# Optimization experiments

Hardware: AMD Instinct MI355X
Metric: run time of the kernel (lower is better)

## Reference

```python
import jax, jax.numpy as jnp
import numpy as np

CH = 64          # channels
OC = 64          # out_channels
B, H, W = 8, 128, 128
NCA_C = CH + OC  # 128, NCA state channels
K = 3            # kernel_size
DILS = (1, 2, 4, 8)
HID = 64         # NCA update hidden
EPS = 1e-5


def setup_inputs() -> dict:
    key = jax.random.key(0)
    ks = jax.random.split(key, 16)
    def n(k, shape, s=0.02):
        return jax.random.normal(k, shape, jnp.float32) * s
    return {
        "x": jax.random.normal(ks[0], (B, H, W, CH), jnp.float32),
        "c": jax.random.normal(ks[1], (B, OC), jnp.float32),
        # Attention params
        "Wq": n(ks[2], (CH, OC)), "bq": jnp.zeros((OC,), jnp.float32),
        "Wk": n(ks[3], (OC, OC)), "bk": jnp.zeros((OC,), jnp.float32),
        "Wv": n(ks[4], (OC, OC)), "bv": jnp.zeros((OC,), jnp.float32),
        "Wo": n(ks[5], (OC, OC)), "bo": jnp.zeros((OC,), jnp.float32),
        "ln_g": jnp.ones((OC,), jnp.float32), "ln_b": jnp.zeros((OC,), jnp.float32),
        # NCA depthwise perception kernels, one per dilation: [4, NCA_C, 1, K, K]
        "pk": n(ks[6], (len(DILS), NCA_C, 1, K, K), 0.1),
        # NCA update MLP
        "W1": n(ks[7], ((1 + len(DILS)) * NCA_C, HID)), "b1": jnp.zeros((HID,), jnp.float32),
        "W2": n(ks[8], (HID, CH)), "b2": jnp.zeros((CH,), jnp.float32),
    }


def _layernorm(z, g, b):
    m = jnp.mean(z, axis=-1, keepdims=True)
    v = jnp.var(z, axis=-1, keepdims=True)
    return (z - m) / jnp.sqrt(v + EPS) * g + b


def _forward(x, c, Wq, bq, Wk, bk, Wv, bv, Wo, bo, ln_g, ln_b, pk, W1, b1, W2, b2):
    b_, h_, w_, _ = x.shape
    # ---- Attention(x, c): single-key softmax pooling over H*W ----
    q = x.reshape(b_, h_ * w_, CH) @ Wq + bq              # [B, HW, OC]
    k = c @ Wk + bk                                        # [B, OC]
    v = c @ Wv + bv                                        # [B, OC]
    scores = jnp.einsum('bno,bo->bn', q, k) * (OC ** -0.5)  # [B, HW]
    attn = jax.nn.softmax(scores, axis=1)                  # softmax over spatial dim
    attended = jnp.einsum('bn,bo->bo', attn, v)            # weighted pool (weights sum to 1)
    a = _layernorm(attended @ Wo + bo + c, ln_g, ln_b)     # out_proj + residual + LN
    c2 = c + a                                             # outer residual in NCAAttention

    # ---- concat broadcast context -> NCA state [B,H,W,NCA_C] ----
    c_exp = jnp.broadcast_to(c2[:, None, None, :], (b_, h_, w_, OC))
    xc = jnp.concatenate([x, c_exp], axis=-1)

    # ---- NCA perception: depthwise dilated convs (SAME padding) ----
    xp = jnp.transpose(xc, (0, 3, 1, 2))                   # NCHW
    feats = [xc]
    for i, d in enumerate(DILS):
        pad = d * (K // 2)
        p = jax.lax.conv_general_dilated(
            xp, pk[i], window_strides=(1, 1),
            padding=[(pad, pad), (pad, pad)], rhs_dilation=(d, d),
            dimension_numbers=('NCHW', 'OIHW', 'NCHW'),
            feature_group_count=NCA_C)
        feats.append(jnp.transpose(p, (0, 2, 3, 1)))
    upd_in = jnp.concatenate(feats, axis=-1)               # [B,H,W,5*NCA_C]

    # ---- NCA update MLP: Linear -> (Dropout=id) -> GELU -> Linear ----
    hidden = jax.nn.gelu(upd_in @ W1 + b1, approximate=False)
    y = hidden @ W2 + b2                                   # [B,H,W,CH]
    # NCA.out_channels (64) != NCA.channels (128) -> no residual add
    return y, c2


def reference(x, c, Wq, bq, Wk, bk, Wv, bv, Wo, bo, ln_g, ln_b, pk, W1, b1, W2, b2):
    return _forward(x, c, Wq, bq, Wk, bk, Wv, bv, Wo, bo, ln_g, ln_b, pk, W1, b1, W2, b2)
```

## Files before the change

kernel.cpp:

```cpp
#include <hip/hip_runtime.h>
#include <hip/hip_bf16.h>
#include <math.h>


typedef float  f32x4 __attribute__((ext_vector_type(4)));
typedef short  s16x8 __attribute__((ext_vector_type(8)));
typedef long   i64x2 __attribute__((ext_vector_type(2)));

static __device__ __forceinline__ unsigned short f2bf(float f) {
    __hip_bfloat16 h = __float2bfloat16(f);
    unsigned short u; __builtin_memcpy(&u, &h, 2); return u;
}
static __device__ __forceinline__ unsigned pk4fp8(float f0, float f1, float f2, float f3) {
    int v = 0;
    v = __builtin_amdgcn_cvt_pk_fp8_f32(f0, f1, v, false);
    v = __builtin_amdgcn_cvt_pk_fp8_f32(f2, f3, v, true);
    return (unsigned)v;
}

#define XROWB  9216
#define XBATCH 1327104
#define USCALE 256.0f

__global__ void prep2(const float* __restrict__ x,  const float* __restrict__ pk,
                      const float* __restrict__ W1, const float* __restrict__ W2,
                      const float* __restrict__ b1,
                      const float* __restrict__ c,
                      const float* __restrict__ Wv, const float* __restrict__ bv,
                      const float* __restrict__ Wo, const float* __restrict__ bo,
                      const float* __restrict__ lng, const float* __restrict__ lnb,
                      unsigned char* __restrict__ xp, unsigned char* __restrict__ Uf,
                      unsigned short* __restrict__ W2s,
                      float* __restrict__ V, float* __restrict__ hcp,
                      float* __restrict__ outc2)
{
    const int blk = blockIdx.x, tid = threadIdx.x;
    __shared__ float sc[512], sv[512], c2s[512];

    if (blk >= 683) {
        sc[tid] = c[tid]; sc[tid + 256] = c[tid + 256];
        __syncthreads();
        #pragma unroll
        for (int half = 0; half < 2; ++half) {
            int it = tid + half*256;
            int bb = it >> 6, j = it & 63;
            float v = bv[j];
            for (int i = 0; i < 64; ++i) v += sc[bb*64 + i]*Wv[i*64 + j];
            sv[it] = v;
        }
        __syncthreads();
        #pragma unroll
        for (int half = 0; half < 2; ++half) {
            int it = tid + half*256;
            int bb = it >> 6, j = it & 63;
            float t = bo[j] + sc[it];
            for (int i = 0; i < 64; ++i) t += sv[bb*64 + i]*Wo[i*64 + j];
            float s = t;
            for (int o = 32; o > 0; o >>= 1) s += __shfl_xor(s, o);
            float m = s * (1.f/64.f);
            float dq = (t - m)*(t - m);
            for (int o = 32; o > 0; o >>= 1) dq += __shfl_xor(dq, o);
            float a = (t - m) / sqrtf(dq*(1.f/64.f) + 1e-5f) * lng[j] + lnb[j];
            c2s[it] = sc[it] + a;
        }
        __syncthreads();
    }

    if (blk < 512) {
        int i = blk*256 + tid;
        int xc = i & 127, y = (i >> 7) & 127, b = i >> 14;
        const float* src = x + (size_t)i*64;
        float4 f[16];
        #pragma unroll
        for (int k = 0; k < 16; ++k) f[k] = *(const float4*)(src + k*4);
        unsigned P[16];
        #pragma unroll
        for (int k = 0; k < 16; ++k) P[k] = pk4fp8(f[k].x, f[k].y, f[k].z, f[k].w);
        unsigned char* d = xp + (size_t)b*XBATCH + (size_t)(y+8)*XROWB + (size_t)(xc+8)*64;
        *(uint4*)(d +  0) = make_uint4(P[0], P[1], P[8],  P[9]);
        *(uint4*)(d + 16) = make_uint4(P[2], P[3], P[10], P[11]);
        *(uint4*)(d + 32) = make_uint4(P[4], P[5], P[12], P[13]);
        *(uint4*)(d + 48) = make_uint4(P[6], P[7], P[14], P[15]);
    } else if (blk < 648) {
        int idx = (blk - 512)*256 + tid;
        int b = idx / 4352, r = idx - b*4352;
        int yy, xx;
        if (r < 2304) { int ry = r / 144; xx = r - ry*144; yy = (ry < 8) ? ry : 128 + ry; }
        else { int r2 = r - 2304; yy = 8 + (r2 >> 4); int xi = r2 & 15; xx = (xi < 8) ? xi : 128 + xi; }
        unsigned char* d = xp + (size_t)b*XBATCH + (size_t)yy*XROWB + (size_t)xx*64;
        uint4 z = make_uint4(0,0,0,0);
        *(uint4*)(d) = z; *(uint4*)(d+16) = z; *(uint4*)(d+32) = z; *(uint4*)(d+48) = z;
    } else if (blk < 681) {
        int idx = (blk - 648)*256 + tid;
        if (idx < 8448) {
            int lane = idx & 63, nt = (idx >> 6) & 3, pos = idx >> 8;
            int n  = nt*16 + (lane & 15);
            static constexpr int DI[33] = {3,3,3, 2,2,2, 1,1,1, 0,0,0, -1, 0,0, 1,1, 2,2, 3,3,
                                           0,0,0, 1,1,1, 2,2,2, 3,3,3};
            static constexpr int TT[33] = {0,1,2, 0,1,2, 0,1,2, 0,1,2, 4, 3,5, 3,5, 3,5, 3,5,
                                           6,7,8, 6,7,8, 6,7,8, 6,7,8};
            int di = DI[pos], t = TT[pos];
            float vv[16];
            #pragma unroll
            for (int kc2 = 0; kc2 < 2; ++kc2)
                #pragma unroll
                for (int j = 0; j < 8; ++j) {
                    int ch = kc2*32 + (lane >> 4)*8 + j;
                    float v;
                    if (di < 0) {
                        v = W1[ch*64 + n];
                        for (int dd = 0; dd < 4; ++dd)
                            v += pk[(dd*128 + ch)*9 + 4] * W1[((1+dd)*128 + ch)*64 + n];
                    } else {
                        v = pk[(di*128 + ch)*9 + t] * W1[((1+di)*128 + ch)*64 + n];
                    }
                    vv[kc2*8 + j] = v * USCALE;
                }
            uint4 o;
            o.x = pk4fp8(vv[0],  vv[1],  vv[2],  vv[3]);
            o.y = pk4fp8(vv[4],  vv[5],  vv[6],  vv[7]);
            o.z = pk4fp8(vv[8],  vv[9],  vv[10], vv[11]);
            o.w = pk4fp8(vv[12], vv[13], vv[14], vv[15]);
            *(uint4*)(Uf + (size_t)idx*16) = o;
        }
    } else if (blk < 683) {
        int idx = (blk - 681)*256 + tid;
        int lane = idx & 63, nt = (idx >> 6) & 3, kc2 = (idx >> 8) & 1;
        int n  = nt*16 + (lane & 15);
        int k0 = kc2*32 + (lane >> 4)*8;
        unsigned short e[8];
        #pragma unroll
        for (int j = 0; j < 8; ++j) e[j] = f2bf(W2[(k0+j)*64 + n]);
        uint4 o;
        o.x = (unsigned)e[0] | ((unsigned)e[1] << 16);
        o.y = (unsigned)e[2] | ((unsigned)e[3] << 16);
        o.z = (unsigned)e[4] | ((unsigned)e[5] << 16);
        o.w = (unsigned)e[6] | ((unsigned)e[7] << 16);
        *(uint4*)(W2s + (size_t)idx*8) = o;
    } else if (blk < 755) {
        int idx = (blk - 683)*256 + tid;
        int n = idx & 63, q = idx >> 6;
        int p = q % 36, b = q / 36;
        int di = p/9, t = p%9;
        float s = 0.f;
        for (int j = 0; j < 64; ++j)
            s += c2s[b*64 + j] * pk[(di*128 + 64 + j)*9 + t] * W1[((1+di)*128 + 64 + j)*64 + n];
        V[(size_t)q*64 + n] = s;
    } else {
        for (int it = tid; it < 512; it += 256) {
            int b = it >> 6, n = it & 63;
            float s = b1[n];
            for (int j = 0; j < 64; ++j) s += c2s[b*64 + j]*W1[(64 + j)*64 + n];
            hcp[it] = s;
            if (blk == 755) outc2[it] = c2s[it];
        }
    }
}

#define HID_S 72

__global__ __launch_bounds__(512, 4) void nca_main(
    const unsigned char* __restrict__ xp,
    const unsigned char* __restrict__ U,
    const unsigned short* __restrict__ W2s,
    const float* __restrict__ V,
    const float* __restrict__ hcp,
    const float* __restrict__ b2,
    float* __restrict__ out)
{
    __shared__ __align__(16) unsigned char smem[36864];
    __shared__ float V_l[36*64];
    __shared__ float Cx_l[16*64];
    __shared__ float Cy_l[2*64];
    __shared__ float hc2_l[64];

    unsigned short* hid = (unsigned short*)smem;

    const int tid = threadIdx.x;
    const int blk = blockIdx.x;
    const int b  = blk & 7;
    const int y0 = (blk >> 3) * 2;

    #pragma unroll
    for (int s = 0; s < 2; ++s) {
        int off = tid*16 + s*8192;
        __builtin_amdgcn_global_load_lds(
            (const __attribute__((address_space(1))) unsigned int*)(U + off),
            (__attribute__((address_space(3))) unsigned int*)(smem + off),
            16, 0, 0);
    }

    {
        const float4* Vg = (const float4*)(V + (size_t)b*2304);
        for (int i = tid; i < 576; i += 512) ((float4*)V_l)[i] = Vg[i];
    }
    __syncthreads();
    for (int it = tid; it < 1024; it += 512) {
        int xi = it >> 6, n = it & 63;
        int xx = xi < 8 ? xi : 112 + xi;
        float s = 0.f;
        #pragma unroll
        for (int di = 0; di < 4; ++di) {
            int d = 1 << di;
            int dxo = (xx < d) ? 0 : ((xx >= 128 - d) ? 2 : -1);
            if (dxo >= 0) {
                s += V_l[(di*9 + 0*3 + dxo)*64 + n];
                s += V_l[(di*9 + 1*3 + dxo)*64 + n];
                s += V_l[(di*9 + 2*3 + dxo)*64 + n];
            }
        }
        Cx_l[it] = s;
    }
    if (tid < 128) {
        int r = tid >> 6, n = tid & 63;
        int yy = y0 + r;
        float s = 0.f;
        #pragma unroll
        for (int di = 0; di < 4; ++di) {
            int d = 1 << di;
            int dyo = (yy < d) ? 0 : ((yy >= 128 - d) ? 2 : -1);
            if (dyo >= 0) {
                s += V_l[(di*9 + dyo*3 + 0)*64 + n];
                s += V_l[(di*9 + dyo*3 + 1)*64 + n];
                s += V_l[(di*9 + dyo*3 + 2)*64 + n];
            }
        }
        Cy_l[tid] = s;
    } else if (tid < 192) {
        int n = tid - 128;
        float s = hcp[b*64 + n];
        for (int p = 0; p < 36; ++p) s += V_l[p*64 + n];
        hc2_l[n] = s;
    }
    __syncthreads();

    const int lane = tid & 63;
    const int w    = tid >> 6;
    const int rib  = w >> 2;
    const int y    = y0 + rib;
    const int xw   = (w & 3) * 32;
    const int ln15 = lane & 15;
    const int oct  = lane >> 4;

    const unsigned char* abase = xp + (size_t)b*XBATCH + (size_t)(y + 8)*XROWB
                               + (size_t)(xw + ln15 + 8)*64 + oct*16;

    f32x4 acc[2][4];
    #pragma unroll
    for (int mt = 0; mt < 2; ++mt)
        #pragma unroll
        for (int nt = 0; nt < 4; ++nt) {
            acc[mt][nt][0] = 0.f; acc[mt][nt][1] = 0.f;
            acc[mt][nt][2] = 0.f; acc[mt][nt][3] = 0.f;
        }

    static constexpr int OFF[33] = {
        (-8*144-8)*64, (-8*144)*64, (-8*144+8)*64,
        (-4*144-4)*64, (-4*144)*64, (-4*144+4)*64,
        (-2*144-2)*64, (-2*144)*64, (-2*144+2)*64,
        (-1*144-1)*64, (-1*144)*64, (-1*144+1)*64,
        0,
        -64, 64, -128, 128, -256, 256, -512, 512,
        ( 1*144-1)*64, ( 1*144)*64, ( 1*144+1)*64,
        ( 2*144-2)*64, ( 2*144)*64, ( 2*144+2)*64,
        ( 4*144-4)*64, ( 4*144)*64, ( 4*144+4)*64,
        ( 8*144-8)*64, ( 8*144)*64, ( 8*144+8)*64
    };

    auto loadA = [&](int pos, i64x2* A) {
        const unsigned char* rp = abase + OFF[pos];
        A[0] = *(const i64x2*)(rp);
        A[1] = *(const i64x2*)(rp + 1024);
    };
    auto loadB = [&](int bufofs, int p, i64x2* Bv) {
        const unsigned char* rp = smem + bufofs + p*4096 + lane*16;
        #pragma unroll
        for (int nt = 0; nt < 4; ++nt) Bv[nt] = *(const i64x2*)(rp + nt*1024);
    };
    auto mfma_step = [&](const i64x2* A, const i64x2* Bv) {
        #pragma unroll
        for (int kc2 = 0; kc2 < 2; ++kc2)
            #pragma unroll
            for (int nt = 0; nt < 4; ++nt) {
                long bfr = Bv[nt][kc2];
                #pragma unroll
                for (int mt = 0; mt < 2; ++mt)
                    acc[mt][nt] = __builtin_amdgcn_mfma_f32_16x16x32_fp8_fp8(A[mt][kc2], bfr, acc[mt][nt], 0, 0, 0);
            }
    };

    i64x2 Areg[2][2], Breg[2][4];
    loadA(0, Areg[0]);
    loadB(0, 0, Breg[0]);

    int cur = 0;
    #pragma unroll 1
    for (int kb = 0; kb < 8; ++kb) {
        {
            const int nbytes = (kb < 7) ? 16384 : 4096;
            const unsigned char* gsrc = U + (size_t)(kb + 1)*16384;
            unsigned char* ldst = smem + (cur ^ 1)*16384;
            for (int off = tid*16; off < nbytes; off += 8192)
                __builtin_amdgcn_global_load_lds(
                    (const __attribute__((address_space(1))) unsigned int*)(gsrc + off),
                    (__attribute__((address_space(3))) unsigned int*)(ldst + off),
                    16, 0, 0);
        }
        const int cofs = cur*16384;
        #pragma unroll
        for (int p = 0; p < 4; ++p) {
            const int pos = kb*4 + p;
            loadA(pos + 1, Areg[(p + 1) & 1]);
            if (p < 3) loadB(cofs, p + 1, Breg[(p + 1) & 1]);
            __builtin_amdgcn_s_setprio(1);
            mfma_step(Areg[p & 1], Breg[p & 1]);
            __builtin_amdgcn_s_setprio(0);
        }
        __syncthreads();
        cur ^= 1;
        loadB(cur*16384, 0, Breg[0]);
    }
    __builtin_amdgcn_s_setprio(1);
    mfma_step(Areg[0], Breg[0]);
    __builtin_amdgcn_s_setprio(0);
    __syncthreads();

    const bool yedge = (y < 8) || (y >= 120);
    #pragma unroll
    for (int mt = 0; mt < 2; ++mt) {
        #pragma unroll
        for (int nt = 0; nt < 4; ++nt) {
            const int n = nt*16 + ln15;
            const float hcv = hc2_l[n];
            const float cyv = yedge ? Cy_l[rib*64 + n] : 0.f;
            #pragma unroll
            for (int r = 0; r < 4; ++r) {
                int m = oct*4 + r;
                int x = xw + mt*16 + m;
                float h = acc[mt][nt][r]*(1.0f/USCALE) + hcv - cyv;
                if (x < 8 || x >= 120) {
                    int xi = (x < 8) ? x : (x - 112);
                    h -= Cx_l[xi*64 + n];
                    if (yedge) {
                        #pragma unroll
                        for (int di = 0; di < 4; ++di) {
                            int d = 1 << di;
                            int dyo = (y < d) ? 0 : ((y >= 128 - d) ? 2 : -1);
                            int dxo = (x < d) ? 0 : ((x >= 128 - d) ? 2 : -1);
                            if (dyo >= 0 && dxo >= 0)
                                h += V_l[(di*9 + dyo*3 + dxo)*64 + n];
                        }
                    }
                }
                float u = 0.7978845608028654f * (h + 0.044715f*h*h*h);
                float g = h / (1.f + __expf(-2.f*u));
                hid[(rib*128 + x)*HID_S + n] = f2bf(g);
            }
        }
    }

    f32x4 acc2[2][4];
    #pragma unroll
    for (int mt = 0; mt < 2; ++mt)
        #pragma unroll
        for (int nt = 0; nt < 4; ++nt) {
            acc2[mt][nt][0] = 0.f; acc2[mt][nt][1] = 0.f;
            acc2[mt][nt][2] = 0.f; acc2[mt][nt][3] = 0.f;
        }
    #pragma unroll
    for (int kc2 = 0; kc2 < 2; ++kc2) {
        s16x8 a2[2];
        #pragma unroll
        for (int mt = 0; mt < 2; ++mt)
            a2[mt] = *(const s16x8*)&hid[(rib*128 + xw + mt*16 + ln15)*HID_S + kc2*32 + oct*8];
        #pragma unroll
        for (int nt = 0; nt < 4; ++nt) {
            s16x8 bfr = *(const s16x8*)(W2s + ((size_t)(kc2*4 + nt)*64 + lane)*8);
            #pragma unroll
            for (int mt = 0; mt < 2; ++mt)
                acc2[mt][nt] = __builtin_amdgcn_mfma_f32_16x16x32_bf16(a2[mt], bfr, acc2[mt][nt], 0, 0, 0);
        }
    }

    float* ob = out + ((size_t)(b*128 + y))*128*64;
    #pragma unroll
    for (int nt = 0; nt < 4; ++nt) {
        const float b2v = b2[nt*16 + ln15];
        #pragma unroll
        for (int mt = 0; mt < 2; ++mt) {
            #pragma unroll
            for (int r = 0; r < 4; ++r) {
                int x = xw + mt*16 + oct*4 + r;
                ob[(size_t)x*64 + nt*16 + ln15] = acc2[mt][nt][r] + b2v;
            }
        }
    }
}

extern "C" void kernel_launch(void* const* d_in, const int* in_sizes, int n_in,
                              void* d_out, int out_size, void* d_ws, size_t ws_size,
                              hipStream_t stream) {
    const float* x   = (const float*)d_in[0];
    const float* c   = (const float*)d_in[1];
    const float* Wv  = (const float*)d_in[6];
    const float* bv  = (const float*)d_in[7];
    const float* Wo  = (const float*)d_in[8];
    const float* bo  = (const float*)d_in[9];
    const float* lng = (const float*)d_in[10];
    const float* lnb = (const float*)d_in[11];
    const float* pk  = (const float*)d_in[12];
    const float* W1  = (const float*)d_in[13];
    const float* b1  = (const float*)d_in[14];
    const float* W2  = (const float*)d_in[15];
    const float* b2  = (const float*)d_in[16];
    float* out = (float*)d_out;

    char* w = (char*)d_ws;
    unsigned char*  xpb = (unsigned char*)(w);
    unsigned char*  Uf  = (unsigned char*)(w + 10616832);
    unsigned short* W2s = (unsigned short*)(w + 10752000);
    float*          V   = (float*)         (w + 10760192);
    float*          hcp = (float*)         (w + 10833920);

    prep2<<<757, 256, 0, stream>>>(x, pk, W1, W2, b1, c, Wv, bv, Wo, bo, lng, lnb,
                                   xpb, Uf, W2s, V, hcp, out + 8388608);
    nca_main<<<512, 512, 0, stream>>>(xpb, Uf, W2s, V, hcp, b2, out);
}
```

Measured before the change: 154.5 us.

## Switch NCA main GEMM to 32x32x64 scaled FP8 MFMA with repacked weights

Replaces the 16x16x32 fp8 MFMA tiles in the first MLP GEMM with the gfx950 32x32x64 f8f6f4 scaled MFMA. The weight U is repacked in the prep kernel for the new operand layout, and the LDS double buffer grows to 32KB stages so the K loop runs 4 iterations instead of 8. The activation staging is changed to coalesced per-channel-group writes. The intent is fewer MFMA issues and fewer LDS/global load instructions per FLOP. In exchange, the larger LDS footprint (64KB) may reduce occupancy.

```diff
diff --git a/kernel.cpp b/kernel.cpp
--- a/kernel.cpp
+++ b/kernel.cpp
@@ -3,9 +3,11 @@
 #include <math.h>
 
 
-typedef float  f32x4 __attribute__((ext_vector_type(4)));
-typedef short  s16x8 __attribute__((ext_vector_type(8)));
-typedef long   i64x2 __attribute__((ext_vector_type(2)));
+typedef float  f32x4  __attribute__((ext_vector_type(4)));
+typedef float  f32x16 __attribute__((ext_vector_type(16)));
+typedef short  s16x8  __attribute__((ext_vector_type(8)));
+typedef int    i32x4  __attribute__((ext_vector_type(4)));
+typedef int    i32x8  __attribute__((ext_vector_type(8)));
 
 static __device__ __forceinline__ unsigned short f2bf(float f) {
     __hip_bfloat16 h = __float2bfloat16(f);
@@ -37,7 +39,7 @@
     const int blk = blockIdx.x, tid = threadIdx.x;
     __shared__ float sc[512], sv[512], c2s[512];
 
-    if (blk >= 683) {
+    if (blk >= 667) {
         sc[tid] = c[tid]; sc[tid + 256] = c[tid + 256];
         __syncthreads();
         #pragma unroll
@@ -67,20 +69,16 @@
     }
 
     if (blk < 512) {
-        int i = blk*256 + tid;
-        int xc = i & 127, y = (i >> 7) & 127, b = i >> 14;
-        const float* src = x + (size_t)i*64;
-        float4 f[16];
-        #pragma unroll
-        for (int k = 0; k < 16; ++k) f[k] = *(const float4*)(src + k*4);
-        unsigned P[16];
-        #pragma unroll
-        for (int k = 0; k < 16; ++k) P[k] = pk4fp8(f[k].x, f[k].y, f[k].z, f[k].w);
-        unsigned char* d = xp + (size_t)b*XBATCH + (size_t)(y+8)*XROWB + (size_t)(xc+8)*64;
-        *(uint4*)(d +  0) = make_uint4(P[0], P[1], P[8],  P[9]);
-        *(uint4*)(d + 16) = make_uint4(P[2], P[3], P[10], P[11]);
-        *(uint4*)(d + 32) = make_uint4(P[4], P[5], P[12], P[13]);
-        *(uint4*)(d + 48) = make_uint4(P[6], P[7], P[14], P[15]);
+        const int ci = tid & 15;
+        #pragma unroll 4
+        for (int it = 0; it < 16; ++it) {
+            int px = blk*256 + it*16 + (tid >> 4);
+            int xc = px & 127, y = (px >> 7) & 127, b = px >> 14;
+            float4 f = *(const float4*)(x + (size_t)px*64 + ci*4);
+            unsigned P = pk4fp8(f.x, f.y, f.z, f.w);
+            *(unsigned*)(xp + (size_t)b*XBATCH + (size_t)(y+8)*XROWB
+                            + (size_t)(xc+8)*64 + ci*4) = P;
+        }
     } else if (blk < 648) {
         int idx = (blk - 512)*256 + tid;
         int b = idx / 4352, r = idx - b*4352;
@@ -90,41 +88,46 @@
         unsigned char* d = xp + (size_t)b*XBATCH + (size_t)yy*XROWB + (size_t)xx*64;
         uint4 z = make_uint4(0,0,0,0);
         *(uint4*)(d) = z; *(uint4*)(d+16) = z; *(uint4*)(d+32) = z; *(uint4*)(d+48) = z;
-    } else if (blk < 681) {
+    } else if (blk < 665) {
         int idx = (blk - 648)*256 + tid;
-        if (idx < 8448) {
-            int lane = idx & 63, nt = (idx >> 6) & 3, pos = idx >> 8;
-            int n  = nt*16 + (lane & 15);
+        if (idx < 4224) {
+            int lane = idx & 63, nt = (idx >> 6) & 1, pos = idx >> 7;
+            int n  = nt*32 + (lane & 31);
+            int h  = lane >> 5;
             static constexpr int DI[33] = {3,3,3, 2,2,2, 1,1,1, 0,0,0, -1, 0,0, 1,1, 2,2, 3,3,
                                            0,0,0, 1,1,1, 2,2,2, 3,3,3};
             static constexpr int TT[33] = {0,1,2, 0,1,2, 0,1,2, 0,1,2, 4, 3,5, 3,5, 3,5, 3,5,
                                            6,7,8, 6,7,8, 6,7,8, 6,7,8};
             int di = DI[pos], t = TT[pos];
-            float vv[16];
+            float vv[32];
             #pragma unroll
-            for (int kc2 = 0; kc2 < 2; ++kc2)
-                #pragma unroll
-                for (int j = 0; j < 8; ++j) {
-                    int ch = kc2*32 + (lane >> 4)*8 + j;
-                    float v;
-                    if (di < 0) {
-                        v = W1[ch*64 + n];
-                        for (int dd = 0; dd < 4; ++dd)
-                            v += pk[(dd*128 + ch)*9 + 4] * W1[((1+dd)*128 + ch)*64 + n];
-                    } else {
-                        v = pk[(di*128 + ch)*9 + t] * W1[((1+di)*128 + ch)*64 + n];
-                    }
-                    vv[kc2*8 + j] = v * USCALE;
+            for (int j = 0; j < 32; ++j) {
+                int ch = h*32 + j;
+                float v;
+                if (di < 0) {
+                    v = W1[ch*64 + n];
+                    for (int dd = 0; dd < 4; ++dd)
+                        v += pk[(dd*128 + ch)*9 + 4] * W1[((1+dd)*128 + ch)*64 + n];
+                } else {
+                    v = pk[(di*128 + ch)*9 + t] * W1[((1+di)*128 + ch)*64 + n];
                 }
-            uint4 o;
-            o.x = pk4fp8(vv[0],  vv[1],  vv[2],  vv[3]);
-            o.y = pk4fp8(vv[4],  vv[5],  vv[6],  vv[7]);
-            o.z = pk4fp8(vv[8],  vv[9],  vv[10], vv[11]);
-            o.w = pk4fp8(vv[12], vv[13], vv[14], vv[15]);
-            *(uint4*)(Uf + (size_t)idx*16) = o;
-        }
-    } else if (blk < 683) {
-        int idx = (blk - 681)*256 + tid;
+                vv[j] = v * USCALE;
+            }
+            unsigned char* base = Uf + (size_t)pos*4096 + nt*2048 + lane*16;
+            uint4 o0, o1;
+            o0.x = pk4fp8(vv[0],  vv[1],  vv[2],  vv[3]);
+            o0.y = pk4fp8(vv[4],  vv[5],  vv[6],  vv[7]);
+            o0.z = pk4fp8(vv[8],  vv[9],  vv[10], vv[11]);
+            o0.w = pk4fp8(vv[12], vv[13], vv[14], vv[15]);
+            o1.x = pk4fp8(vv[16], vv[17], vv[18], vv[19]);
+            o1.y = pk4fp8(vv[20], vv[21], vv[22], vv[23]);
+            o1.z = pk4fp8(vv[24], vv[25], vv[26], vv[27]);
+            o1.w = pk4fp8(vv[28], vv[29], vv[30], vv[31]);
+            *(uint4*)(base)        = o0;
+            *(uint4*)(base + 1024) = o1;
+        }
+    } else if (blk < 667) {
+        int idx = (blk - 665)*256 + tid;
         int lane = idx & 63, nt = (idx >> 6) & 3, kc2 = (idx >> 8) & 1;
         int n  = nt*16 + (lane & 15);
         int k0 = kc2*32 + (lane >> 4)*8;
@@ -137,8 +140,8 @@
         o.z = (unsigned)e[4] | ((unsigned)e[5] << 16);
         o.w = (unsigned)e[6] | ((unsigned)e[7] << 16);
         *(uint4*)(W2s + (size_t)idx*8) = o;
-    } else if (blk < 755) {
-        int idx = (blk - 683)*256 + tid;
+    } else if (blk < 739) {
+        int idx = (blk - 667)*256 + tid;
         int n = idx & 63, q = idx >> 6;
         int p = q % 36, b = q / 36;
         int di = p/9, t = p%9;
@@ -152,7 +155,7 @@
             float s = b1[n];
             for (int j = 0; j < 64; ++j) s += c2s[b*64 + j]*W1[(64 + j)*64 + n];
             hcp[it] = s;
-            if (blk == 755) outc2[it] = c2s[it];
+            outc2[it] = c2s[it];
         }
     }
 }
@@ -168,7 +171,7 @@
     const float* __restrict__ b2,
     float* __restrict__ out)
 {
-    __shared__ __align__(16) unsigned char smem[36864];
+    __shared__ __align__(16) unsigned char smem[65536];
     __shared__ float V_l[36*64];
     __shared__ float Cx_l[16*64];
     __shared__ float Cy_l[2*64];
@@ -182,7 +185,7 @@
     const int y0 = (blk >> 3) * 2;
 
     #pragma unroll
-    for (int s = 0; s < 2; ++s) {
+    for (int s = 0; s < 4; ++s) {
         int off = tid*16 + s*8192;
         __builtin_amdgcn_global_load_lds(
             (const __attribute__((address_space(1))) unsigned int*)(U + off),
@@ -241,18 +244,17 @@
     const int xw   = (w & 3) * 32;
     const int ln15 = lane & 15;
     const int oct  = lane >> 4;
+    const int l31  = lane & 31;
+    const int kg   = lane >> 5;
 
     const unsigned char* abase = xp + (size_t)b*XBATCH + (size_t)(y + 8)*XROWB
-                               + (size_t)(xw + ln15 + 8)*64 + oct*16;
-
-    f32x4 acc[2][4];
-    #pragma unroll
-    for (int mt = 0; mt < 2; ++mt)
-        #pragma unroll
-        for (int nt = 0; nt < 4; ++nt) {
-            acc[mt][nt][0] = 0.f; acc[mt][nt][1] = 0.f;
-            acc[mt][nt][2] = 0.f; acc[mt][nt][3] = 0.f;
-        }
+                               + (size_t)(xw + l31 + 8)*64 + kg*32;
+
+    f32x16 acc[2];
+    #pragma unroll
+    for (int nt = 0; nt < 2; ++nt)
+        #pragma unroll
+        for (int r = 0; r < 16; ++r) acc[nt][r] = 0.f;
 
     static constexpr int OFF[33] = {
         (-8*144-8)*64, (-8*144)*64, (-8*144+8)*64,
@@ -267,95 +269,90 @@
         ( 8*144-8)*64, ( 8*144)*64, ( 8*144+8)*64
     };
 
-    auto loadA = [&](int pos, i64x2* A) {
-        const unsigned char* rp = abase + OFF[pos];
-        A[0] = *(const i64x2*)(rp);
-        A[1] = *(const i64x2*)(rp + 1024);
+    auto loadB = [&](int cofs, int p, i32x8* Bv) {
+        const unsigned char* rp = smem + cofs + p*4096 + lane*16;
+        #pragma unroll
+        for (int nt = 0; nt < 2; ++nt) {
+            i32x4 lo = *(const i32x4*)(rp + nt*2048);
+            i32x4 hi = *(const i32x4*)(rp + nt*2048 + 1024);
+            i32x8 v;
+            v[0]=lo[0]; v[1]=lo[1]; v[2]=lo[2]; v[3]=lo[3];
+            v[4]=hi[0]; v[5]=hi[1]; v[6]=hi[2]; v[7]=hi[3];
+            Bv[nt] = v;
+        }
     };
-    auto loadB = [&](int bufofs, int p, i64x2* Bv) {
-        const unsigned char* rp = smem + bufofs + p*4096 + lane*16;
-        #pragma unroll
-        for (int nt = 0; nt < 4; ++nt) Bv[nt] = *(const i64x2*)(rp + nt*1024);
-    };
-    auto mfma_step = [&](const i64x2* A, const i64x2* Bv) {
-        #pragma unroll
-        for (int kc2 = 0; kc2 < 2; ++kc2)
-            #pragma unroll
-            for (int nt = 0; nt < 4; ++nt) {
-                long bfr = Bv[nt][kc2];
-                #pragma unroll
-                for (int mt = 0; mt < 2; ++mt)
-                    acc[mt][nt] = __builtin_amdgcn_mfma_f32_16x16x32_fp8_fp8(A[mt][kc2], bfr, acc[mt][nt], 0, 0, 0);
-            }
-    };
-
-    i64x2 Areg[2][2], Breg[2][4];
-    loadA(0, Areg[0]);
+
+    i32x8 Areg[2];
+    i32x8 Breg[2][2];
+    Areg[0] = *(const i32x8*)(abase + OFF[0]);
     loadB(0, 0, Breg[0]);
 
     int cur = 0;
     #pragma unroll 1
-    for (int kb = 0; kb < 8; ++kb) {
+    for (int kb = 0; kb < 4; ++kb) {
         {
-            const int nbytes = (kb < 7) ? 16384 : 4096;
-            const unsigned char* gsrc = U + (size_t)(kb + 1)*16384;
-            unsigned char* ldst = smem + (cur ^ 1)*16384;
+            const int nbytes = (kb < 3) ? 32768 : 4096;
+            const unsigned char* gsrc = U + (size_t)(kb + 1)*32768;
+            unsigned char* ldst = smem + (cur ^ 1)*32768;
             for (int off = tid*16; off < nbytes; off += 8192)
                 __builtin_amdgcn_global_load_lds(
                     (const __attribute__((address_space(1))) unsigned int*)(gsrc + off),
                     (__attribute__((address_space(3))) unsigned int*)(ldst + off),
                     16, 0, 0);
         }
-        const int cofs = cur*16384;
-        #pragma unroll
-        for (int p = 0; p < 4; ++p) {
-            const int pos = kb*4 + p;
-            loadA(pos + 1, Areg[(p + 1) & 1]);
-            if (p < 3) loadB(cofs, p + 1, Breg[(p + 1) & 1]);
+        const int cofs = cur*32768;
+        #pragma unroll
+        for (int p = 0; p < 8; ++p) {
+            const int pos = kb*8 + p;
+            Areg[(p + 1) & 1] = *(const i32x8*)(abase + OFF[pos + 1]);
+            if (p < 7) loadB(cofs, p + 1, Breg[(p + 1) & 1]);
             __builtin_amdgcn_s_setprio(1);
-            mfma_step(Areg[p & 1], Breg[p & 1]);
+            acc[0] = __builtin_amdgcn_mfma_scale_f32_32x32x64_f8f6f4(
+                Areg[p & 1], Breg[p & 1][0], acc[0], 0, 0, 0, 0x7F7F7F7F, 0, 0x7F7F7F7F);
+            acc[1] = __builtin_amdgcn_mfma_scale_f32_32x32x64_f8f6f4(
+                Areg[p & 1], Breg[p & 1][1], acc[1], 0, 0, 0, 0x7F7F7F7F, 0, 0x7F7F7F7F);
             __builtin_amdgcn_s_setprio(0);
         }
         __syncthreads();
         cur ^= 1;
-        loadB(cur*16384, 0, Breg[0]);
+        loadB(cur*32768, 0, Breg[0]);
     }
     __builtin_amdgcn_s_setprio(1);
-    mfma_step(Areg[0], Breg[0]);
+    acc[0] = __builtin_amdgcn_mfma_scale_f32_32x32x64_f8f6f4(
+        Areg[0], Breg[0][0], acc[0], 0, 0, 0, 0x7F7F7F7F, 0, 0x7F7F7F7F);
+    acc[1] = __builtin_amdgcn_mfma_scale_f32_32x32x64_f8f6f4(
+        Areg[0], Breg[0][1], acc[1], 0, 0, 0, 0x7F7F7F7F, 0, 0x7F7F7F7F);
     __builtin_amdgcn_s_setprio(0);
     __syncthreads();
 
     const bool yedge = (y < 8) || (y >= 120);
     #pragma unroll
-    for (int mt = 0; mt < 2; ++mt) {
-        #pragma unroll
-        for (int nt = 0; nt < 4; ++nt) {
-            const int n = nt*16 + ln15;
-            const float hcv = hc2_l[n];
-            const float cyv = yedge ? Cy_l[rib*64 + n] : 0.f;
-            #pragma unroll
-            for (int r = 0; r < 4; ++r) {
-                int m = oct*4 + r;
-                int x = xw + mt*16 + m;
-                float h = acc[mt][nt][r]*(1.0f/USCALE) + hcv - cyv;
-                if (x < 8 || x >= 120) {
-                    int xi = (x < 8) ? x : (x - 112);
-                    h -= Cx_l[xi*64 + n];
-                    if (yedge) {
-                        #pragma unroll
-                        for (int di = 0; di < 4; ++di) {
-                            int d = 1 << di;
-                            int dyo = (y < d) ? 0 : ((y >= 128 - d) ? 2 : -1);
-                            int dxo = (x < d) ? 0 : ((x >= 128 - d) ? 2 : -1);
-                            if (dyo >= 0 && dxo >= 0)
-                                h += V_l[(di*9 + dyo*3 + dxo)*64 + n];
-                        }
+    for (int nt = 0; nt < 2; ++nt) {
+        const int n = nt*32 + l31;
+        const float hcv = hc2_l[n];
+        const float cyv = yedge ? Cy_l[rib*64 + n] : 0.f;
+        #pragma unroll
+        for (int reg = 0; reg < 16; ++reg) {
+            int row = (reg & 3) + 8*(reg >> 2) + 4*kg;
+            int x = xw + row;
+            float h = acc[nt][reg]*(1.0f/USCALE) + hcv - cyv;
+            if (x < 8 || x >= 120) {
+                int xi = (x < 8) ? x : (x - 112);
+                h -= Cx_l[xi*64 + n];
+                if (yedge) {
+                    #pragma unroll
+                    for (int di = 0; di < 4; ++di) {
+                        int d = 1 << di;
+                        int dyo = (y < d) ? 0 : ((y >= 128 - d) ? 2 : -1);
+                        int dxo = (x < d) ? 0 : ((x >= 128 - d) ? 2 : -1);
+                        if (dyo >= 0 && dxo >= 0)
+                            h += V_l[(di*9 + dyo*3 + dxo)*64 + n];
                     }
                 }
-                float u = 0.7978845608028654f * (h + 0.044715f*h*h*h);
-                float g = h / (1.f + __expf(-2.f*u));
-                hid[(rib*128 + x)*HID_S + n] = f2bf(g);
             }
+            float u = 0.7978845608028654f * (h + 0.044715f*h*h*h);
+            float g = h / (1.f + __expf(-2.f*u));
+            hid[(rib*128 + x)*HID_S + n] = f2bf(g);
         }
     }
 
@@ -422,7 +419,7 @@
     float*          V   = (float*)         (w + 10760192);
     float*          hcp = (float*)         (w + 10833920);
 
-    prep2<<<757, 256, 0, stream>>>(x, pk, W1, W2, b1, c, Wv, bv, Wo, bo, lng, lnb,
+    prep2<<<740, 256, 0, stream>>>(x, pk, W1, W2, b1, c, Wv, bv, Wo, bo, lng, lnb,
                                    xpb, Uf, W2s, V, hcp, out + 8388608);
     nca_main<<<512, 512, 0, stream>>>(xpb, Uf, W2s, V, hcp, b2, out);
 }
```

Result: faster. 150.3 us (-2.7%).
